# Kernel tuning notes

Hardware: AMD Instinct MI355X
Metric: run time of the kernel (lower is better)

Reference implementation:

```python
import jax, jax.numpy as jnp
import numpy as np

B, A, D, E = 32, 1024, 384, 4   # batch, atoms, descriptor dim, n_elements
H1, H2 = 256, 192               # n_hidden = [256, 192]


def setup_inputs() -> dict:
    key = jax.random.key(0)
    ks = jax.random.split(key, 8)
    representation = jax.random.normal(ks[0], (B, A, D), dtype=jnp.float32)
    species = jax.random.randint(ks[1], (B, A), 0, E, dtype=jnp.int32)
    s = 0.05
    W1 = jax.random.normal(ks[2], (E, D, H1), dtype=jnp.float32) * s
    b1 = jax.random.normal(ks[3], (E, H1), dtype=jnp.float32) * s
    Wh = jax.random.normal(ks[4], (E, H1, H2), dtype=jnp.float32) * s
    bh = jax.random.normal(ks[5], (E, H2), dtype=jnp.float32) * s
    W2 = jax.random.normal(ks[6], (E, H2), dtype=jnp.float32) * s
    b2 = jax.random.normal(ks[7], (E,), dtype=jnp.float32) * s
    return {"representation": representation, "species": species,
            "W1": W1, "b1": b1, "Wh": Wh, "bh": bh, "W2": W2, "b2": b2}


def reference(representation, species, W1, b1, Wh, bh, W2, b2):
    # Dense compute of ALL element nets for every atom (faithful to torch code).
    # MLP: layer1 output is NOT activated (quirk of the original forward);
    # activation only applies to the intermediate `layers` list entries.
    h = jnp.einsum('bad,edh->baeh', representation, W1) + b1          # [B,A,E,H1]
    h = jax.nn.relu(jnp.einsum('baeh,ehk->baek', h, Wh) + bh)         # [B,A,E,H2]
    element_energies = jnp.einsum('baek,ek->bae', h, W2) + b2         # [B,A,E]
    onehot = jax.nn.one_hot(species, E, dtype=element_energies.dtype) # [B,A,E]
    energies = jnp.sum(onehot * element_energies, axis=(1, 2))        # [B]
    return energies
```

## Files before the change

### kernel.cpp

```cpp
#include <hip/hip_runtime.h>

typedef __attribute__((ext_vector_type(8))) short bf16x8;
typedef __attribute__((ext_vector_type(4))) float f32x4;
typedef unsigned short ushort_t;

#define NB 32
#define NA 1024
#define NATOMS (NB*NA)
#define D  384
#define H1 256
#define H2 192
#define NE 4
#define TA 64
#define NGRID 515

#define XLD 40
#define HLD 264

__device__ __forceinline__ ushort_t f2bf(float f) {
    union { float f; unsigned u; } v; v.f = f;
    unsigned r = v.u + 0x7FFF + ((v.u >> 16) & 1);
    return (ushort_t)(r >> 16);
}

__global__ void zero_kernel(int* __restrict__ counts) {
    if (threadIdx.x < NE) counts[threadIdx.x] = 0;
}

__global__ __launch_bounds__(256) void scatter_kernel(
    const int* __restrict__ species, int* __restrict__ counts, int* __restrict__ bucket)
{
    __shared__ int wcnt[4][4];
    __shared__ int wbase[4][4];
    const int t = threadIdx.x, lane = t & 63, wv = t >> 6;
    const int i = blockIdx.x * 256 + t;
    const int e = species[i];

    unsigned long long m0 = __ballot(e == 0);
    unsigned long long m1 = __ballot(e == 1);
    unsigned long long m2 = __ballot(e == 2);
    unsigned long long m3 = __ballot(e == 3);
    unsigned long long mym = (e == 0) ? m0 : (e == 1) ? m1 : (e == 2) ? m2 : m3;
    const unsigned long long lt = (lane == 63) ? 0x7FFFFFFFFFFFFFFFull
                                               : ((1ull << lane) - 1ull);
    const int rank = __popcll(mym & lt);

    if (lane == 0) {
        wcnt[wv][0] = __popcll(m0); wcnt[wv][1] = __popcll(m1);
        wcnt[wv][2] = __popcll(m2); wcnt[wv][3] = __popcll(m3);
    }
    __syncthreads();
    if (t < NE) {
        int s = t;
        int tot = wcnt[0][s] + wcnt[1][s] + wcnt[2][s] + wcnt[3][s];
        int b = atomicAdd(&counts[s], tot);
        for (int w = 0; w < 4; ++w) { wbase[w][s] = b; b += wcnt[w][s]; }
    }
    __syncthreads();
    bucket[(e << 15) + wbase[wv][e] + rank] = i;
}

__global__ __launch_bounds__(256) void transpose_kernel(
    const float* __restrict__ W1, const float* __restrict__ Wh,
    ushort_t* __restrict__ w1t, ushort_t* __restrict__ wht)
{
    __shared__ float tile[32][33];
    const int t = threadIdx.x;
    int bid = blockIdx.x;
    const float* src; ushort_t* dst; int R, C, e, rt, ct;
    if (bid < NE * 96) {
        e = bid / 96; int rem = bid % 96; rt = rem / 8; ct = rem % 8;
        src = W1; dst = w1t; R = D; C = H1;
    } else {
        bid -= NE * 96;
        e = bid / 48; int rem = bid % 48; rt = rem / 6; ct = rem % 6;
        src = Wh; dst = wht; R = H1; C = H2;
    }
    const float* S  = src + ((size_t)e * R + rt * 32) * C + ct * 32;
    ushort_t*    Dp = dst + ((size_t)e * C + ct * 32) * R + rt * 32;
    {
        int row = t >> 3, c4 = (t & 7) * 4;
        float4 v = *(const float4*)(S + (size_t)row * C + c4);
        tile[row][c4 + 0] = v.x; tile[row][c4 + 1] = v.y;
        tile[row][c4 + 2] = v.z; tile[row][c4 + 3] = v.w;
    }
    __syncthreads();
    {
        int orow = t >> 3, k4 = (t & 7) * 4;
        ushort4 o;
        o.x = f2bf(tile[k4 + 0][orow]);
        o.y = f2bf(tile[k4 + 1][orow]);
        o.z = f2bf(tile[k4 + 2][orow]);
        o.w = f2bf(tile[k4 + 3][orow]);
        *(ushort4*)(Dp + (size_t)orow * R + k4) = o;
    }
}

__global__ __launch_bounds__(256, 3) void mlp_kernel(
    const float*    __restrict__ rep,
    const int*      __restrict__ counts,
    const int*      __restrict__ bucket,
    const ushort_t* __restrict__ w1t,
    const ushort_t* __restrict__ wht,
    const float*    __restrict__ b1,
    const float*    __restrict__ bh,
    const float*    __restrict__ W2,
    const float*    __restrict__ b2,
    float*          __restrict__ energy)
{
    const int c0 = counts[0], c1 = counts[1], c2 = counts[2], c3 = counts[3];
    const int t0 = (c0 + 63) >> 6, t1 = (c1 + 63) >> 6, t2 = (c2 + 63) >> 6, t3 = (c3 + 63) >> 6;
    int bid = blockIdx.x;
    int e, tile, n;
    if      (bid < t0)                { e = 0; tile = bid;                n = c0; }
    else if (bid < t0 + t1)           { e = 1; tile = bid - t0;           n = c1; }
    else if (bid < t0 + t1 + t2)      { e = 2; tile = bid - t0 - t1;      n = c2; }
    else if (bid < t0 + t1 + t2 + t3) { e = 3; tile = bid - t0 - t1 - t2; n = c3; }
    else return;
    const int base = tile * TA;

    const int t    = threadIdx.x;
    const int lane = t & 63;
    const int wv   = t >> 6;
    const int g    = lane >> 4;
    const int r    = lane & 15;

    __shared__ ushort_t Xt[2][TA * XLD];
    __shared__ ushort_t H1t[TA * HLD];
    __shared__ float    eparts[4 * TA];
    __shared__ int      idx_lds[TA];

    if (t < TA)
        idx_lds[t] = (base + t < n) ? bucket[(e << 15) + base + t] : -1;
    __syncthreads();

    const int xrow0 = t >> 3, xrow1 = 32 + xrow0, xc4 = (t & 7) * 4;
    int gi0 = idx_lds[xrow0]; if (gi0 < 0) gi0 = 0;
    int gi1 = idx_lds[xrow1]; if (gi1 < 0) gi1 = 0;
    const float* xp0 = rep + (size_t)gi0 * D + xc4;
    const float* xp1 = rep + (size_t)gi1 * D + xc4;

    const ushort_t* a1p = w1t + ((size_t)e * H1 + wv * 64 + r) * D + g * 8;

    uint4 afc[4], afn[4];
    #pragma unroll
    for (int nn = 0; nn < 4; ++nn)
        afc[nn] = *(const uint4*)(a1p + nn * 16 * D);

    float4 rx0 = *(const float4*)(xp0);
    float4 rx1 = *(const float4*)(xp1);
    {
        ushort4 o;
        o.x = f2bf(rx0.x); o.y = f2bf(rx0.y); o.z = f2bf(rx0.z); o.w = f2bf(rx0.w);
        *(ushort4*)(&Xt[0][xrow0 * XLD + xc4]) = o;
        o.x = f2bf(rx1.x); o.y = f2bf(rx1.y); o.z = f2bf(rx1.z); o.w = f2bf(rx1.w);
        *(ushort4*)(&Xt[0][xrow1 * XLD + xc4]) = o;
    }
    __syncthreads();

    f32x4 acc1[4][4];
    #pragma unroll
    for (int nn = 0; nn < 4; ++nn)
        #pragma unroll
        for (int m = 0; m < 4; ++m)
            acc1[nn][m] = (f32x4){0.f, 0.f, 0.f, 0.f};

    for (int ks = 0; ks < 12; ++ks) {
        const int cur = ks & 1;
        if (ks < 11) {
            const int k0n = (ks + 1) * 32;
            rx0 = *(const float4*)(xp0 + k0n);
            rx1 = *(const float4*)(xp1 + k0n);
            #pragma unroll
            for (int nn = 0; nn < 4; ++nn)
                afn[nn] = *(const uint4*)(a1p + nn * 16 * D + k0n);
        }
        bf16x8 bw[4];
        #pragma unroll
        for (int m = 0; m < 4; ++m)
            bw[m] = *(const bf16x8*)(&Xt[cur][(m * 16 + r) * XLD + g * 8]);
        #pragma unroll
        for (int nn = 0; nn < 4; ++nn)
            #pragma unroll
            for (int m = 0; m < 4; ++m)
                acc1[nn][m] = __builtin_amdgcn_mfma_f32_16x16x32_bf16(
                    __builtin_bit_cast(bf16x8, afc[nn]), bw[m], acc1[nn][m], 0, 0, 0);
        if (ks < 11) {
            ushort4 o;
            o.x = f2bf(rx0.x); o.y = f2bf(rx0.y); o.z = f2bf(rx0.z); o.w = f2bf(rx0.w);
            *(ushort4*)(&Xt[cur ^ 1][xrow0 * XLD + xc4]) = o;
            o.x = f2bf(rx1.x); o.y = f2bf(rx1.y); o.z = f2bf(rx1.z); o.w = f2bf(rx1.w);
            *(ushort4*)(&Xt[cur ^ 1][xrow1 * XLD + xc4]) = o;
            __syncthreads();
            #pragma unroll
            for (int nn = 0; nn < 4; ++nn) afc[nn] = afn[nn];
        }
    }

    float b1v[4][4];
    #pragma unroll
    for (int nn = 0; nn < 4; ++nn)
        #pragma unroll
        for (int q = 0; q < 4; ++q)
            b1v[nn][q] = b1[e * H1 + wv * 64 + nn * 16 + g * 4 + q];

    #pragma unroll
    for (int nn = 0; nn < 4; ++nn)
        #pragma unroll
        for (int m = 0; m < 4; ++m) {
            unsigned p0 = f2bf(acc1[nn][m][0] + b1v[nn][0]);
            unsigned p1 = f2bf(acc1[nn][m][1] + b1v[nn][1]);
            unsigned p2 = f2bf(acc1[nn][m][2] + b1v[nn][2]);
            unsigned p3 = f2bf(acc1[nn][m][3] + b1v[nn][3]);
            uint2 pk; pk.x = p0 | (p1 << 16); pk.y = p2 | (p3 << 16);
            *(uint2*)(&H1t[(m * 16 + r) * HLD + wv * 64 + nn * 16 + g * 4]) = pk;
        }
    __syncthreads();

    const ushort_t* a2p = wht + ((size_t)e * H2 + wv * 48 + r) * H1 + g * 8;

    f32x4 acc2[3][4];
    #pragma unroll
    for (int nn = 0; nn < 3; ++nn)
        #pragma unroll
        for (int m = 0; m < 4; ++m)
            acc2[nn][m] = (f32x4){0.f, 0.f, 0.f, 0.f};

    uint4 af2c[3], af2n[3];
    #pragma unroll
    for (int nn = 0; nn < 3; ++nn)
        af2c[nn] = *(const uint4*)(a2p + nn * 16 * H1);

    for (int ks = 0; ks < 8; ++ks) {
        const int k0 = ks * 32;
        if (ks < 7) {
            #pragma unroll
            for (int nn = 0; nn < 3; ++nn)
                af2n[nn] = *(const uint4*)(a2p + nn * 16 * H1 + k0 + 32);
        }
        bf16x8 bw2[4];
        #pragma unroll
        for (int m = 0; m < 4; ++m)
            bw2[m] = *(const bf16x8*)(&H1t[(m * 16 + r) * HLD + k0 + g * 8]);
        #pragma unroll
        for (int nn = 0; nn < 3; ++nn)
            #pragma unroll
            for (int m = 0; m < 4; ++m)
                acc2[nn][m] = __builtin_amdgcn_mfma_f32_16x16x32_bf16(
                    __builtin_bit_cast(bf16x8, af2c[nn]), bw2[m], acc2[nn][m], 0, 0, 0);
        if (ks < 7) {
            #pragma unroll
            for (int nn = 0; nn < 3; ++nn) af2c[nn] = af2n[nn];
        }
    }

    float bhv[3][4], w2v[3][4];
    #pragma unroll
    for (int nn = 0; nn < 3; ++nn)
        #pragma unroll
        for (int q = 0; q < 4; ++q) {
            int h2i = e * H2 + wv * 48 + nn * 16 + g * 4 + q;
            bhv[nn][q] = bh[h2i];
            w2v[nn][q] = W2[h2i];
        }
    const float b2e = b2[e];

    #pragma unroll
    for (int m = 0; m < 4; ++m) {
        float s = 0.f;
        #pragma unroll
        for (int nn = 0; nn < 3; ++nn)
            #pragma unroll
            for (int q = 0; q < 4; ++q) {
                float z = acc2[nn][m][q] + bhv[nn][q];
                z = fmaxf(z, 0.f);
                s += z * w2v[nn][q];
            }
        s += __shfl_xor(s, 16, 64);
        s += __shfl_xor(s, 32, 64);
        if (lane < 16) eparts[wv * TA + m * 16 + r] = s;
    }
    __syncthreads();
    if (t < TA) {
        int gi = idx_lds[t];
        if (gi >= 0)
            energy[gi] = eparts[t] + eparts[TA + t] + eparts[2 * TA + t]
                       + eparts[3 * TA + t] + b2e;
    }
}

__global__ void reduce_kernel(const float* __restrict__ energy, float* __restrict__ out) {
    const int b = blockIdx.x, t = threadIdx.x;
    float s = 0.f;
    for (int i = t; i < NA; i += 256) s += energy[b * NA + i];
    for (int off = 32; off > 0; off >>= 1) s += __shfl_down(s, off, 64);
    __shared__ float ws[4];
    if ((t & 63) == 0) ws[t >> 6] = s;
    __syncthreads();
    if (t == 0) out[b] = ws[0] + ws[1] + ws[2] + ws[3];
}

extern "C" void kernel_launch(void* const* d_in, const int* in_sizes, int n_in,
                              void* d_out, int out_size, void* d_ws, size_t ws_size,
                              hipStream_t stream) {
    const float* rep     = (const float*)d_in[0];
    const int*   species = (const int*)  d_in[1];
    const float* W1      = (const float*)d_in[2];
    const float* b1      = (const float*)d_in[3];
    const float* Wh      = (const float*)d_in[4];
    const float* bh      = (const float*)d_in[5];
    const float* W2      = (const float*)d_in[6];
    const float* b2      = (const float*)d_in[7];
    float* out = (float*)d_out;

    char* ws = (char*)d_ws;
    int*      counts  = (int*)      (ws + 0);
    int*      bucket  = (int*)      (ws + 64);
    float*    energy  = (float*)    (ws + 524352);
    ushort_t* w1t     = (ushort_t*) (ws + 655424);
    ushort_t* wht     = (ushort_t*) (ws + 1441856);

    zero_kernel<<<1, 64, 0, stream>>>(counts);
    scatter_kernel<<<NATOMS / 256, 256, 0, stream>>>(species, counts, bucket);
    transpose_kernel<<<NE * 96 + NE * 48, 256, 0, stream>>>(W1, Wh, w1t, wht);
    mlp_kernel<<<NGRID, 256, 0, stream>>>(rep, counts, bucket, w1t, wht,
                                          b1, bh, W2, b2, energy);
    reduce_kernel<<<NB, 256, 0, stream>>>(energy, out);
}
```

Baseline: 125.5 us.

## Halve atom tile, stage full X tile in swizzled LDS, fold counts zeroing

Cuts the atom tile from 64 to 32, doubling the grid so more blocks run per CU, and raises the occupancy hint. The whole bf16 X tile (32x384) is now loaded into LDS up front with an XOR swizzle instead of double-buffered 32-column slices, which removes the per-k-step barriers. Weights are read straight from global memory inside the unrolled loops rather than register-prefetched. The zero kernel is merged into the transpose kernel, saving one launch. Each weight fragment is now reused across only 2 MFMA columns instead of 4, so weight traffic through L2 doubles.

Result: slower. 142.1 us (+13.2%).

```diff
diff --git a/kernel.cpp b/kernel.cpp
--- a/kernel.cpp
+++ b/kernel.cpp
@@ -11,20 +11,13 @@
 #define H1 256
 #define H2 192
 #define NE 4
-#define TA 64
-#define NGRID 515
-
-#define XLD 40
-#define HLD 264
+#define TA 32
+#define NGRID 1027
 
 __device__ __forceinline__ ushort_t f2bf(float f) {
     union { float f; unsigned u; } v; v.f = f;
     unsigned r = v.u + 0x7FFF + ((v.u >> 16) & 1);
     return (ushort_t)(r >> 16);
-}
-
-__global__ void zero_kernel(int* __restrict__ counts) {
-    if (threadIdx.x < NE) counts[threadIdx.x] = 0;
 }
 
 __global__ __launch_bounds__(256) void scatter_kernel(
@@ -62,8 +55,10 @@
 
 __global__ __launch_bounds__(256) void transpose_kernel(
     const float* __restrict__ W1, const float* __restrict__ Wh,
-    ushort_t* __restrict__ w1t, ushort_t* __restrict__ wht)
+    ushort_t* __restrict__ w1t, ushort_t* __restrict__ wht,
+    int* __restrict__ counts)
 {
+    if (blockIdx.x == 0 && threadIdx.x < NE) counts[threadIdx.x] = 0;
     __shared__ float tile[32][33];
     const int t = threadIdx.x;
     int bid = blockIdx.x;
@@ -96,7 +91,7 @@
     }
 }
 
-__global__ __launch_bounds__(256, 3) void mlp_kernel(
+__global__ __launch_bounds__(256, 4) void mlp_kernel(
     const float*    __restrict__ rep,
     const int*      __restrict__ counts,
     const int*      __restrict__ bucket,
@@ -109,7 +104,8 @@
     float*          __restrict__ energy)
 {
     const int c0 = counts[0], c1 = counts[1], c2 = counts[2], c3 = counts[3];
-    const int t0 = (c0 + 63) >> 6, t1 = (c1 + 63) >> 6, t2 = (c2 + 63) >> 6, t3 = (c3 + 63) >> 6;
+    const int t0 = (c0 + 31) >> 5, t1 = (c1 + 31) >> 5, t2 = (c2 + 31) >> 5;
+    const int t3 = (c3 + 31) >> 5;
     int bid = blockIdx.x;
     int e, tile, n;
     if      (bid < t0)                { e = 0; tile = bid;                n = c0; }
@@ -124,168 +120,142 @@
     const int wv   = t >> 6;
     const int g    = lane >> 4;
     const int r    = lane & 15;
-
-    __shared__ ushort_t Xt[2][TA * XLD];
-    __shared__ ushort_t H1t[TA * HLD];
-    __shared__ float    eparts[4 * TA];
-    __shared__ int      idx_lds[TA];
-
-    if (t < TA)
-        idx_lds[t] = (base + t < n) ? bucket[(e << 15) + base + t] : -1;
-    __syncthreads();
-
-    const int xrow0 = t >> 3, xrow1 = 32 + xrow0, xc4 = (t & 7) * 4;
-    int gi0 = idx_lds[xrow0]; if (gi0 < 0) gi0 = 0;
-    int gi1 = idx_lds[xrow1]; if (gi1 < 0) gi1 = 0;
-    const float* xp0 = rep + (size_t)gi0 * D + xc4;
-    const float* xp1 = rep + (size_t)gi1 * D + xc4;
+    const int r7   = r & 7;
+
+    __shared__ ushort_t smem[TA * D + TA * H1];
+    ushort_t* Xt  = smem;
+    ushort_t* H1t = smem + TA * D;
+    float*    eparts = (float*)smem;
+
+    {
+        const int srow = t >> 3, scs = t & 7, sswz = srow & 7;
+        int ai = base + srow;
+        int gs = bucket[(e << 15) + (ai < n ? ai : base)];
+        const float* xp = rep + (size_t)gs * D;
+        #pragma unroll
+        for (int i = 0; i < 6; ++i) {
+            const int cs = scs + 8 * i;
+            float4 v0 = *(const float4*)(xp + cs * 8);
+            float4 v1 = *(const float4*)(xp + cs * 8 + 4);
+            union { bf16x8 v; ushort_t u[8]; } pk;
+            pk.u[0] = f2bf(v0.x); pk.u[1] = f2bf(v0.y);
+            pk.u[2] = f2bf(v0.z); pk.u[3] = f2bf(v0.w);
+            pk.u[4] = f2bf(v1.x); pk.u[5] = f2bf(v1.y);
+            pk.u[6] = f2bf(v1.z); pk.u[7] = f2bf(v1.w);
+            *(bf16x8*)(Xt + srow * D + ((cs ^ sswz) << 3)) = pk.v;
+        }
+    }
+    __syncthreads();
 
     const ushort_t* a1p = w1t + ((size_t)e * H1 + wv * 64 + r) * D + g * 8;
 
-    uint4 afc[4], afn[4];
+    f32x4 acc1[4][2];
     #pragma unroll
     for (int nn = 0; nn < 4; ++nn)
-        afc[nn] = *(const uint4*)(a1p + nn * 16 * D);
-
-    float4 rx0 = *(const float4*)(xp0);
-    float4 rx1 = *(const float4*)(xp1);
-    {
-        ushort4 o;
-        o.x = f2bf(rx0.x); o.y = f2bf(rx0.y); o.z = f2bf(rx0.z); o.w = f2bf(rx0.w);
-        *(ushort4*)(&Xt[0][xrow0 * XLD + xc4]) = o;
-        o.x = f2bf(rx1.x); o.y = f2bf(rx1.y); o.z = f2bf(rx1.z); o.w = f2bf(rx1.w);
-        *(ushort4*)(&Xt[0][xrow1 * XLD + xc4]) = o;
-    }
-    __syncthreads();
-
-    f32x4 acc1[4][4];
-    #pragma unroll
-    for (int nn = 0; nn < 4; ++nn)
-        #pragma unroll
-        for (int m = 0; m < 4; ++m)
+        #pragma unroll
+        for (int m = 0; m < 2; ++m)
             acc1[nn][m] = (f32x4){0.f, 0.f, 0.f, 0.f};
 
+    #pragma unroll 4
     for (int ks = 0; ks < 12; ++ks) {
-        const int cur = ks & 1;
-        if (ks < 11) {
-            const int k0n = (ks + 1) * 32;
-            rx0 = *(const float4*)(xp0 + k0n);
-            rx1 = *(const float4*)(xp1 + k0n);
+        bf16x8 bx[2];
+        #pragma unroll
+        for (int m = 0; m < 2; ++m) {
+            const int cs = ks * 4 + g;
+            bx[m] = *(const bf16x8*)(Xt + (m * 16 + r) * D + ((cs ^ r7) << 3));
+        }
+        #pragma unroll
+        for (int nn = 0; nn < 4; ++nn) {
+            bf16x8 aw = *(const bf16x8*)(a1p + (size_t)nn * 16 * D + ks * 32);
             #pragma unroll
-            for (int nn = 0; nn < 4; ++nn)
-                afn[nn] = *(const uint4*)(a1p + nn * 16 * D + k0n);
-        }
-        bf16x8 bw[4];
-        #pragma unroll
-        for (int m = 0; m < 4; ++m)
-            bw[m] = *(const bf16x8*)(&Xt[cur][(m * 16 + r) * XLD + g * 8]);
-        #pragma unroll
-        for (int nn = 0; nn < 4; ++nn)
+            for (int m = 0; m < 2; ++m)
+                acc1[nn][m] = __builtin_amdgcn_mfma_f32_16x16x32_bf16(
+                    aw, bx[m], acc1[nn][m], 0, 0, 0);
+        }
+    }
+
+    #pragma unroll
+    for (int nn = 0; nn < 4; ++nn) {
+        float bv[4];
+        #pragma unroll
+        for (int q = 0; q < 4; ++q)
+            bv[q] = b1[e * H1 + wv * 64 + nn * 16 + g * 4 + q];
+        #pragma unroll
+        for (int m = 0; m < 2; ++m) {
+            unsigned p0 = f2bf(acc1[nn][m][0] + bv[0]);
+            unsigned p1 = f2bf(acc1[nn][m][1] + bv[1]);
+            unsigned p2 = f2bf(acc1[nn][m][2] + bv[2]);
+            unsigned p3 = f2bf(acc1[nn][m][3] + bv[3]);
+            uint2 pk; pk.x = p0 | (p1 << 16); pk.y = p2 | (p3 << 16);
+            const int col = wv * 64 + nn * 16 + g * 4;
+            const int cs  = col >> 3;
+            const int phys = (m * 16 + r) * H1 + ((cs ^ r7) << 3) + (col & 7);
+            *(uint2*)(H1t + phys) = pk;
+        }
+    }
+    __syncthreads();
+
+    const ushort_t* a2p = wht + ((size_t)e * H2 + wv * 48 + r) * H1 + g * 8;
+
+    f32x4 acc2[3][2];
+    #pragma unroll
+    for (int nn = 0; nn < 3; ++nn)
+        #pragma unroll
+        for (int m = 0; m < 2; ++m)
+            acc2[nn][m] = (f32x4){0.f, 0.f, 0.f, 0.f};
+
+    #pragma unroll 4
+    for (int ks = 0; ks < 8; ++ks) {
+        bf16x8 bx[2];
+        #pragma unroll
+        for (int m = 0; m < 2; ++m) {
+            const int cs = ks * 4 + g;
+            bx[m] = *(const bf16x8*)(H1t + (m * 16 + r) * H1 + ((cs ^ r7) << 3));
+        }
+        #pragma unroll
+        for (int nn = 0; nn < 3; ++nn) {
+            bf16x8 aw = *(const bf16x8*)(a2p + (size_t)nn * 16 * H1 + ks * 32);
             #pragma unroll
-            for (int m = 0; m < 4; ++m)
-                acc1[nn][m] = __builtin_amdgcn_mfma_f32_16x16x32_bf16(
-                    __builtin_bit_cast(bf16x8, afc[nn]), bw[m], acc1[nn][m], 0, 0, 0);
-        if (ks < 11) {
-            ushort4 o;
-            o.x = f2bf(rx0.x); o.y = f2bf(rx0.y); o.z = f2bf(rx0.z); o.w = f2bf(rx0.w);
-            *(ushort4*)(&Xt[cur ^ 1][xrow0 * XLD + xc4]) = o;
-            o.x = f2bf(rx1.x); o.y = f2bf(rx1.y); o.z = f2bf(rx1.z); o.w = f2bf(rx1.w);
-            *(ushort4*)(&Xt[cur ^ 1][xrow1 * XLD + xc4]) = o;
-            __syncthreads();
-            #pragma unroll
-            for (int nn = 0; nn < 4; ++nn) afc[nn] = afn[nn];
-        }
-    }
-
-    float b1v[4][4];
-    #pragma unroll
-    for (int nn = 0; nn < 4; ++nn)
-        #pragma unroll
-        for (int q = 0; q < 4; ++q)
-            b1v[nn][q] = b1[e * H1 + wv * 64 + nn * 16 + g * 4 + q];
-
-    #pragma unroll
-    for (int nn = 0; nn < 4; ++nn)
-        #pragma unroll
-        for (int m = 0; m < 4; ++m) {
-            unsigned p0 = f2bf(acc1[nn][m][0] + b1v[nn][0]);
-            unsigned p1 = f2bf(acc1[nn][m][1] + b1v[nn][1]);
-            unsigned p2 = f2bf(acc1[nn][m][2] + b1v[nn][2]);
-            unsigned p3 = f2bf(acc1[nn][m][3] + b1v[nn][3]);
-            uint2 pk; pk.x = p0 | (p1 << 16); pk.y = p2 | (p3 << 16);
-            *(uint2*)(&H1t[(m * 16 + r) * HLD + wv * 64 + nn * 16 + g * 4]) = pk;
-        }
-    __syncthreads();
-
-    const ushort_t* a2p = wht + ((size_t)e * H2 + wv * 48 + r) * H1 + g * 8;
-
-    f32x4 acc2[3][4];
-    #pragma unroll
-    for (int nn = 0; nn < 3; ++nn)
-        #pragma unroll
-        for (int m = 0; m < 4; ++m)
-            acc2[nn][m] = (f32x4){0.f, 0.f, 0.f, 0.f};
-
-    uint4 af2c[3], af2n[3];
-    #pragma unroll
-    for (int nn = 0; nn < 3; ++nn)
-        af2c[nn] = *(const uint4*)(a2p + nn * 16 * H1);
-
-    for (int ks = 0; ks < 8; ++ks) {
-        const int k0 = ks * 32;
-        if (ks < 7) {
-            #pragma unroll
-            for (int nn = 0; nn < 3; ++nn)
-                af2n[nn] = *(const uint4*)(a2p + nn * 16 * H1 + k0 + 32);
-        }
-        bf16x8 bw2[4];
-        #pragma unroll
-        for (int m = 0; m < 4; ++m)
-            bw2[m] = *(const bf16x8*)(&H1t[(m * 16 + r) * HLD + k0 + g * 8]);
-        #pragma unroll
-        for (int nn = 0; nn < 3; ++nn)
-            #pragma unroll
-            for (int m = 0; m < 4; ++m)
+            for (int m = 0; m < 2; ++m)
                 acc2[nn][m] = __builtin_amdgcn_mfma_f32_16x16x32_bf16(
-                    __builtin_bit_cast(bf16x8, af2c[nn]), bw2[m], acc2[nn][m], 0, 0, 0);
-        if (ks < 7) {
-            #pragma unroll
-            for (int nn = 0; nn < 3; ++nn) af2c[nn] = af2n[nn];
-        }
-    }
-
-    float bhv[3][4], w2v[3][4];
-    #pragma unroll
-    for (int nn = 0; nn < 3; ++nn)
+                    aw, bx[m], acc2[nn][m], 0, 0, 0);
+        }
+    }
+
+    float s2[2] = {0.f, 0.f};
+    #pragma unroll
+    for (int nn = 0; nn < 3; ++nn) {
+        float bhv[4], w2v[4];
         #pragma unroll
         for (int q = 0; q < 4; ++q) {
             int h2i = e * H2 + wv * 48 + nn * 16 + g * 4 + q;
-            bhv[nn][q] = bh[h2i];
-            w2v[nn][q] = W2[h2i];
-        }
-    const float b2e = b2[e];
-
-    #pragma unroll
-    for (int m = 0; m < 4; ++m) {
-        float s = 0.f;
-        #pragma unroll
-        for (int nn = 0; nn < 3; ++nn)
+            bhv[q] = bh[h2i];
+            w2v[q] = W2[h2i];
+        }
+        #pragma unroll
+        for (int m = 0; m < 2; ++m)
             #pragma unroll
             for (int q = 0; q < 4; ++q) {
-                float z = acc2[nn][m][q] + bhv[nn][q];
+                float z = acc2[nn][m][q] + bhv[q];
                 z = fmaxf(z, 0.f);
-                s += z * w2v[nn][q];
+                s2[m] += z * w2v[q];
             }
+    }
+    #pragma unroll
+    for (int m = 0; m < 2; ++m) {
+        float s = s2[m];
         s += __shfl_xor(s, 16, 64);
         s += __shfl_xor(s, 32, 64);
         if (lane < 16) eparts[wv * TA + m * 16 + r] = s;
     }
     __syncthreads();
     if (t < TA) {
-        int gi = idx_lds[t];
-        if (gi >= 0)
+        int ai = base + t;
+        if (ai < n) {
+            int gi = bucket[(e << 15) + ai];
             energy[gi] = eparts[t] + eparts[TA + t] + eparts[2 * TA + t]
-                       + eparts[3 * TA + t] + b2e;
+                       + eparts[3 * TA + t] + b2[e];
+        }
     }
 }
 
@@ -320,9 +290,8 @@
     ushort_t* w1t     = (ushort_t*) (ws + 655424);
     ushort_t* wht     = (ushort_t*) (ws + 1441856);
 
-    zero_kernel<<<1, 64, 0, stream>>>(counts);
+    transpose_kernel<<<NE * 96 + NE * 48, 256, 0, stream>>>(W1, Wh, w1t, wht, counts);
     scatter_kernel<<<NATOMS / 256, 256, 0, stream>>>(species, counts, bucket);
-    transpose_kernel<<<NE * 96 + NE * 48, 256, 0, stream>>>(W1, Wh, w1t, wht);
     mlp_kernel<<<NGRID, 256, 0, stream>>>(rep, counts, bucket, w1t, wht,
                                           b1, bh, W2, b2, energy);
     reduce_kernel<<<NB, 256, 0, stream>>>(energy, out);
```
